# Kernel tuning notes

Hardware: AMD Instinct MI355X
Metric: run time of the kernel (lower is better)

Reference implementation:

```python
import jax, jax.numpy as jnp
import numpy as np

BS, N, M, E = 2, 512, 128, 16384
NNODE = BS * N
CI = CO = 32  # fused in-channels (16 skip + 16 upsampled), out-channels per degree


def _ln(x, g, b, eps=1e-5):
    mu = jnp.mean(x, -1, keepdims=True)
    var = jnp.var(x, -1, keepdims=True)
    return (x - mu) / jnp.sqrt(var + eps) * g + b


def reference(h0, h1, uph0, uph1, xyz, xyz_prev, r, basis_00, basis_01, basis_10, basis_11,
              rad_w1, rad_b1, rad_ln1_g, rad_ln1_b, rad_w2, rad_b2, rad_ln2_g, rad_ln2_b,
              rad_w3_00, rad_b3_00, rad_w3_01, rad_b3_01, rad_w3_10, rad_b3_10,
              rad_w3_11, rad_b3_11, self_w0, self_w1,
              norm_ln_g0, norm_ln_b0, norm_w0, norm_b0,
              norm_ln_g1, norm_ln_b1, norm_w1, norm_b1,
              edge_src, edge_dst):
    # ---- three_nn + inverse-squared-distance interpolation (upsample uph) ----
    xb = xyz.reshape(BS, N, 3)
    pb = xyz_prev.reshape(BS, M, 3)
    d2 = jnp.sum((xb[:, :, None, :] - pb[:, None, :, :]) ** 2, -1)  # [BS,N,M]
    neg, idx = jax.lax.top_k(-d2, 3)                                # 3 nearest prev points
    d2_3 = jnp.maximum(-neg, 1e-10)                                 # dist*dist with clamp
    inv = 1.0 / (d2_3 + 1e-8)
    w = inv / jnp.sum(inv, -1, keepdims=True)                       # [BS,N,3]
    w = jax.lax.stop_gradient(w)  # three_nn is a non-differentiable custom op in torch

    def interp(up, skip):
        nC, nF = up.shape[1], up.shape[2]
        flat = up.reshape(BS, M, nC * nF)
        g = jax.vmap(lambda f, i: f[i])(flat, idx)                  # [BS,N,3,nC*nF]
        new = jnp.sum(g * w[..., None], axis=2).reshape(BS * N, nC, nF)
        return jnp.concatenate([new, skip], axis=1)                 # upsampled first, then skip

    f0 = interp(uph0, h0)  # [NNODE, 32, 1]
    f1 = interp(uph1, h1)  # [NNODE, 32, 3]

    # ---- GConvSE3: radial nets (hidden trunk stacked over the 4 (di,do) pairs) ----
    hh = jnp.einsum('poi,ei->peo', rad_w1, r) + rad_b1[:, None, :]
    hh = jax.nn.relu(_ln(hh, rad_ln1_g[:, None, :], rad_ln1_b[:, None, :]))
    hh = jnp.einsum('poi,pei->peo', rad_w2, hh) + rad_b2[:, None, :]
    hh = jax.nn.relu(_ln(hh, rad_ln2_g[:, None, :], rad_ln2_b[:, None, :]))  # [4,E,32]

    def rad_out(p, w3, b3, f):
        y = hh[p] @ w3.T + b3
        return y.reshape(E, CO, CI, f)  # (out, in, freq) per RadialFunc.view

    R00 = rad_out(0, rad_w3_00, rad_b3_00, 1)
    R01 = rad_out(1, rad_w3_01, rad_b3_01, 1)
    R10 = rad_out(2, rad_w3_10, rad_b3_10, 1)
    R11 = rad_out(3, rad_w3_11, rad_b3_11, 3)

    src0 = f0[edge_src]; src1 = f1[edge_src]
    dst0 = f0[edge_dst]; dst1 = f1[edge_dst]

    def pair_msg(R, basis, src):
        # kernel[e,o,mo,c,mi] = sum_f R[e,o,c,f] * basis[e,mo,mi,f]; msg = kernel @ src
        T = jnp.einsum('emnf,ecn->ecmf', basis, src)
        return jnp.einsum('eocf,ecmf->eom', R, T)

    msg0 = pair_msg(R00, basis_00, src0) + pair_msg(R10, basis_10, src1)
    msg1 = pair_msg(R01, basis_01, src0) + pair_msg(R11, basis_11, src1)
    # per-edge self-interaction on the destination features
    msg0 = msg0 + jnp.einsum('oc,ecm->eom', self_w0, dst0)
    msg1 = msg1 + jnp.einsum('oc,ecm->eom', self_w1, dst1)

    deg = jnp.maximum(jax.ops.segment_sum(jnp.ones((E,), msg0.dtype), edge_dst, num_segments=NNODE), 1.0)
    out0 = jax.ops.segment_sum(msg0, edge_dst, num_segments=NNODE) / deg[:, None, None]
    out1 = jax.ops.segment_sum(msg1, edge_dst, num_segments=NNODE) / deg[:, None, None]

    # ---- GNormSE3: norm-gated nonlinearity (LayerNorm -> ReLU -> Linear on norms) ----
    def gnorm(v, g, b, wlin, blin):
        nrm = jnp.maximum(jnp.linalg.norm(v, axis=-1, keepdims=True), 1e-12)
        phase = v / nrm
        t = jax.nn.relu(_ln(nrm[..., 0], g, b)) @ wlin.T + blin
        return t[..., None] * phase

    out0 = gnorm(out0, norm_ln_g0, norm_ln_b0, norm_w0, norm_b0)  # [NNODE,32,1]
    out1 = gnorm(out1, norm_ln_g1, norm_ln_b1, norm_w1, norm_b1)  # [NNODE,32,3]
    return jnp.concatenate([out0, out1], axis=-1)                 # [NNODE,32,4]


def setup_inputs() -> dict:
    key = jax.random.key(0)
    ks = iter(jax.random.split(key, 64))
    def rn(shape, scale=1.0):
        return jax.random.normal(next(ks), shape, dtype=jnp.float32) * scale
    inp = {}
    inp['h0'] = rn((NNODE, 16, 1))
    inp['h1'] = rn((NNODE, 16, 3))
    inp['uph0'] = rn((BS * M, 16, 1))
    inp['uph1'] = rn((BS * M, 16, 3))
    inp['xyz'] = rn((NNODE, 3))
    inp['xyz_prev'] = rn((BS * M, 3))
    inp['r'] = jax.random.uniform(next(ks), (E, 1), dtype=jnp.float32, minval=0.05, maxval=2.0)
    inp['basis_00'] = rn((E, 1, 1, 1))
    inp['basis_01'] = rn((E, 3, 1, 1))
    inp['basis_10'] = rn((E, 1, 3, 1))
    inp['basis_11'] = rn((E, 3, 3, 3))
    inp['rad_w1'] = rn((4, 32, 1))
    inp['rad_b1'] = jnp.zeros((4, 32), jnp.float32)
    inp['rad_ln1_g'] = jnp.ones((4, 32), jnp.float32)
    inp['rad_ln1_b'] = jnp.zeros((4, 32), jnp.float32)
    inp['rad_w2'] = rn((4, 32, 32), 1.0 / np.sqrt(32))
    inp['rad_b2'] = jnp.zeros((4, 32), jnp.float32)
    inp['rad_ln2_g'] = jnp.ones((4, 32), jnp.float32)
    inp['rad_ln2_b'] = jnp.zeros((4, 32), jnp.float32)
    for nm, f in (('00', 1), ('01', 1), ('10', 1), ('11', 3)):
        inp['rad_w3_' + nm] = rn((f * CI * CO, 32), 1.0 / np.sqrt(32))
        inp['rad_b3_' + nm] = jnp.zeros((f * CI * CO,), jnp.float32)
    inp['self_w0'] = rn((CO, CI), 1.0 / np.sqrt(CI))
    inp['self_w1'] = rn((CO, CI), 1.0 / np.sqrt(CI))
    for d in ('0', '1'):
        inp['norm_ln_g' + d] = jnp.ones((CO,), jnp.float32)
        inp['norm_ln_b' + d] = jnp.zeros((CO,), jnp.float32)
        inp['norm_w' + d] = rn((CO, CO), 1.0 / np.sqrt(CO))
        inp['norm_b' + d] = jnp.zeros((CO,), jnp.float32)
    inp['edge_src'] = jax.random.randint(next(ks), (E,), 0, NNODE, dtype=jnp.int32)
    inp['edge_dst'] = jax.random.randint(next(ks), (E,), 0, NNODE, dtype=jnp.int32)
    return inp
```

## Files before the change

kernel.cpp:

```cpp
#include <hip/hip_runtime.h>

#define NNODE 1024
#define NPT   512
#define MPT   128
#define ETOT  16384


__global__ void zero_kernel(float* __restrict__ p) {
    const int i = blockIdx.x * 256 + threadIdx.x;
    if (i < 33024) ((float4*)p)[i] = make_float4(0.f, 0.f, 0.f, 0.f);
}

__global__ void interp_kernel(const float* __restrict__ h0, const float* __restrict__ h1,
                              const float* __restrict__ uph0, const float* __restrict__ uph1,
                              const float* __restrict__ xyz, const float* __restrict__ xyzp,
                              float* __restrict__ f0, float* __restrict__ f1) {
    __shared__ float sd2[128];
    __shared__ float sw[3];
    __shared__ int   sidx[3];
    const int n = blockIdx.x;
    const int t = threadIdx.x;
    const int b = n >> 9;
    const float x = xyz[n*3+0], y = xyz[n*3+1], z = xyz[n*3+2];
    const float* pb = &xyzp[(b*MPT + t)*3];
    const float dx = x - pb[0], dy = y - pb[1], dz = z - pb[2];
    sd2[t] = dx*dx + dy*dy + dz*dz;
    __syncthreads();
    if (t == 0) {
        float bd0 = 3.4e38f, bd1 = 3.4e38f, bd2 = 3.4e38f;
        int   i0 = 0, i1 = 0, i2 = 0;
        for (int i = 0; i < 128; ++i) {
            const float d = sd2[i];
            if (d < bd0)      { bd2 = bd1; i2 = i1; bd1 = bd0; i1 = i0; bd0 = d; i0 = i; }
            else if (d < bd1) { bd2 = bd1; i2 = i1; bd1 = d;   i1 = i; }
            else if (d < bd2) { bd2 = d;   i2 = i; }
        }
        const float inv0 = 1.f / (fmaxf(bd0, 1e-10f) + 1e-8f);
        const float inv1 = 1.f / (fmaxf(bd1, 1e-10f) + 1e-8f);
        const float inv2 = 1.f / (fmaxf(bd2, 1e-10f) + 1e-8f);
        const float s = inv0 + inv1 + inv2;
        sw[0] = inv0 / s; sw[1] = inv1 / s; sw[2] = inv2 / s;
        sidx[0] = i0; sidx[1] = i1; sidx[2] = i2;
    }
    __syncthreads();
    const float w0 = sw[0], w1 = sw[1], w2 = sw[2];
    const int g0 = b*MPT + sidx[0], g1 = b*MPT + sidx[1], g2 = b*MPT + sidx[2];
    if (t < 32) {
        const int c = t;
        float v;
        if (c < 16) v = w0*uph0[g0*16+c] + w1*uph0[g1*16+c] + w2*uph0[g2*16+c];
        else        v = h0[n*16 + (c-16)];
        f0[n*32 + c] = v;
    } else {
        const int q = t - 32, c = q / 3, m = q - c*3;
        float v;
        if (c < 16) v = w0*uph1[(g0*16+c)*3+m] + w1*uph1[(g1*16+c)*3+m] + w2*uph1[(g2*16+c)*3+m];
        else        v = h1[(n*16 + (c-16))*3 + m];
        f1[n*96 + c*3 + m] = v;
    }
}

__global__ void trunk_kernel(const float* __restrict__ r,
                             const float* __restrict__ w1, const float* __restrict__ b1,
                             const float* __restrict__ g1, const float* __restrict__ be1,
                             const float* __restrict__ w2, const float* __restrict__ b2,
                             const float* __restrict__ g2, const float* __restrict__ be2,
                             float* __restrict__ hh) {
    const int tid = blockIdx.x * 256 + threadIdx.x;
    const int p = tid >> 14, e = tid & 16383;
    const float rv = r[e];
    float a[32];
    float mu = 0.f;
    #pragma unroll
    for (int o = 0; o < 32; ++o) { a[o] = w1[p*32+o]*rv + b1[p*32+o]; mu += a[o]; }
    mu *= (1.f/32.f);
    float var = 0.f;
    #pragma unroll
    for (int o = 0; o < 32; ++o) { const float d = a[o]-mu; var += d*d; }
    var *= (1.f/32.f);
    float rs = 1.f / sqrtf(var + 1e-5f);
    float h[32];
    #pragma unroll
    for (int o = 0; o < 32; ++o)
        h[o] = fmaxf((a[o]-mu)*rs*g1[p*32+o] + be1[p*32+o], 0.f);
    float a2[32];
    mu = 0.f;
    #pragma unroll
    for (int o = 0; o < 32; ++o) {
        float acc = b2[p*32+o];
        const float* wr = &w2[(p*32+o)*32];
        #pragma unroll
        for (int i = 0; i < 32; ++i) acc += wr[i]*h[i];
        a2[o] = acc; mu += acc;
    }
    mu *= (1.f/32.f);
    var = 0.f;
    #pragma unroll
    for (int o = 0; o < 32; ++o) { const float d = a2[o]-mu; var += d*d; }
    var *= (1.f/32.f);
    rs = 1.f / sqrtf(var + 1e-5f);
    float outv[32];
    #pragma unroll
    for (int o = 0; o < 32; ++o)
        outv[o] = fmaxf((a2[o]-mu)*rs*g2[p*32+o] + be2[p*32+o], 0.f);
    float4* hv = (float4*)&hh[tid*32];
    #pragma unroll
    for (int j = 0; j < 8; ++j)
        hv[j] = make_float4(outv[j*4+0], outv[j*4+1], outv[j*4+2], outv[j*4+3]);
}

struct SmemMsg {
    float w3[32*132];
    float b3[32*5];
    float hh[32*36];
    float src0[32*36];
    float src1[32*100];
    float bas11[32*28];
    float T10[32*33];
    float T11[32*13];
    float bas00[32];
    float bas01[96];
    float bas10[96];
    int   dst[32];
};

template<int P>
__device__ __forceinline__ void process_pair(SmemMsg& sm, const float* __restrict__ hhg,
                                             const float* __restrict__ w3, const float* __restrict__ b3g,
                                             int e0, int tid, int o, int et,
                                             float (&msg0)[4], float (&msg1)[4][3],
                                             const float (&b00r)[4]) {
    constexpr int RPO = (P == 3) ? 96 : 32;
    __syncthreads();
    {
        const int i = tid >> 3, q = tid & 7;
        ((float4*)&sm.hh[i*36])[q] = ((const float4*)&hhg[((P << 14) + e0 + i)*32])[q];
    }
    __syncthreads();
    float4 hhr[4][8];
    #pragma unroll
    for (int ei = 0; ei < 4; ++ei)
        #pragma unroll
        for (int kq = 0; kq < 8; ++kq)
            hhr[ei][kq] = *(const float4*)&sm.hh[(et*4+ei)*36 + kq*4];
    float S01[4] = {0.f, 0.f, 0.f, 0.f};
    constexpr int NCH = RPO / 4;
    #pragma unroll 1
    for (int ch = 0; ch < NCH; ++ch) {
        const int r0 = ch*4;
        __syncthreads();
        {
            const int oo = tid >> 3, hq = tid & 7, rr = hq >> 1, hf = hq & 1;
            const int jrow = oo*RPO + r0 + rr;
            const float4* gs = (const float4*)&w3[jrow*32 + hf*16];
            float4* ld = (float4*)&sm.w3[oo*132 + rr*32 + hf*16];
            #pragma unroll
            for (int j = 0; j < 4; ++j) ld[j] = gs[j];
            if (hq < 4) sm.b3[oo*5 + hq] = b3g[oo*RPO + r0 + hq];
        }
        if (P == 3 && tid < 128) {
            const int e = tid >> 2, rr = tid & 3;
            const int cf = r0 + rr, c = cf / 3, fi = cf - c*3;
            #pragma unroll
            for (int m = 0; m < 3; ++m)
                sm.T11[e*13 + rr*3 + m] =
                      sm.bas11[e*28 + m*9 + 0 + fi] * sm.src1[e*100 + c*3 + 0]
                    + sm.bas11[e*28 + m*9 + 3 + fi] * sm.src1[e*100 + c*3 + 1]
                    + sm.bas11[e*28 + m*9 + 6 + fi] * sm.src1[e*100 + c*3 + 2];
        }
        __syncthreads();
        #pragma unroll
        for (int rr = 0; rr < 4; ++rr) {
            const int row = r0 + rr;
            float4 w[8];
            #pragma unroll
            for (int kq = 0; kq < 8; ++kq)
                w[kq] = *(const float4*)&sm.w3[o*132 + rr*32 + kq*4];
            const float bias = sm.b3[o*5 + rr];
            #pragma unroll
            for (int ei = 0; ei < 4; ++ei) {
                const int eL = et*4 + ei;
                float a0 = bias, a1 = 0.f, a2 = 0.f, a3 = 0.f;
                #pragma unroll
                for (int kq = 0; kq < 8; ++kq) {
                    a0 += w[kq].x * hhr[ei][kq].x;
                    a1 += w[kq].y * hhr[ei][kq].y;
                    a2 += w[kq].z * hhr[ei][kq].z;
                    a3 += w[kq].w * hhr[ei][kq].w;
                }
                const float R = (a0 + a1) + (a2 + a3);
                if (P == 0)      msg0[ei] += R * (b00r[ei] * sm.src0[eL*36 + row]);
                else if (P == 1) S01[ei]  += R * sm.src0[eL*36 + row];
                else if (P == 2) msg0[ei] += R * sm.T10[eL*33 + row];
                else {
                    #pragma unroll
                    for (int m = 0; m < 3; ++m)
                        msg1[ei][m] += R * sm.T11[eL*13 + rr*3 + m];
                }
            }
        }
    }
    if (P == 1) {
        #pragma unroll
        for (int ei = 0; ei < 4; ++ei)
            #pragma unroll
            for (int m = 0; m < 3; ++m)
                msg1[ei][m] += S01[ei] * sm.bas01[(et*4+ei)*3 + m];
    }
}

__launch_bounds__(256, 2)
__global__ void msg_kernel(const float* __restrict__ hhg,
                           const float* __restrict__ f0g, const float* __restrict__ f1g,
                           const float* __restrict__ w00, const float* __restrict__ b00g,
                           const float* __restrict__ w01, const float* __restrict__ b01g,
                           const float* __restrict__ w10, const float* __restrict__ b10g,
                           const float* __restrict__ w11, const float* __restrict__ b11g,
                           const float* __restrict__ bas00g, const float* __restrict__ bas01g,
                           const float* __restrict__ bas10g, const float* __restrict__ bas11g,
                           const int* __restrict__ esrc, const int* __restrict__ edst,
                           float* __restrict__ acc0, float* __restrict__ acc1,
                           float* __restrict__ deg) {
    __shared__ SmemMsg sm;
    const int tid = threadIdx.x;
    const int o = tid & 31, et = tid >> 5;
    const int e0 = blockIdx.x * 32;
    {
        const int i = tid >> 3, q = tid & 7;
        const int eg = e0 + i;
        const int s = esrc[eg];
        ((float4*)&sm.src0[i*36])[q] = ((const float4*)&f0g[s*32])[q];
        #pragma unroll
        for (int j = 0; j < 3; ++j)
            ((float4*)&sm.src1[i*100])[q + 8*j] = ((const float4*)&f1g[s*96])[q + 8*j];
        #pragma unroll
        for (int j = 0; j < 4; ++j) {
            const int idx = q*4 + j;
            if (idx < 27) sm.bas11[i*28 + idx] = bas11g[eg*27 + idx];
        }
        if (q == 0) sm.bas00[i] = bas00g[eg];
        if (q == 1) sm.dst[i] = edst[eg];
        if (q < 3)  sm.bas01[i*3 + q] = bas01g[eg*3 + q];
        if (q >= 4 && q < 7) sm.bas10[i*3 + q - 4] = bas10g[eg*3 + q - 4];
    }
    __syncthreads();
    if (tid < 32) atomicAdd(&deg[sm.dst[tid]], 1.0f);
    {
        #pragma unroll
        for (int j = 0; j < 4; ++j) {
            const int id = tid + 256*j;
            const int e = id >> 5, c = id & 31;
            sm.T10[e*33 + c] = sm.bas10[e*3+0]*sm.src1[e*100 + c*3 + 0]
                             + sm.bas10[e*3+1]*sm.src1[e*100 + c*3 + 1]
                             + sm.bas10[e*3+2]*sm.src1[e*100 + c*3 + 2];
        }
    }
    float msg0[4] = {0.f, 0.f, 0.f, 0.f};
    float msg1[4][3] = {{0,0,0},{0,0,0},{0,0,0},{0,0,0}};
    float b00r[4];
    #pragma unroll
    for (int ei = 0; ei < 4; ++ei) b00r[ei] = sm.bas00[et*4 + ei];

    process_pair<0>(sm, hhg, w00, b00g, e0, tid, o, et, msg0, msg1, b00r);
    process_pair<1>(sm, hhg, w01, b01g, e0, tid, o, et, msg0, msg1, b00r);
    process_pair<2>(sm, hhg, w10, b10g, e0, tid, o, et, msg0, msg1, b00r);
    process_pair<3>(sm, hhg, w11, b11g, e0, tid, o, et, msg0, msg1, b00r);

    #pragma unroll
    for (int ei = 0; ei < 4; ++ei) {
        const int d = sm.dst[et*4 + ei];
        atomicAdd(&acc0[d*32 + o], msg0[ei]);
        #pragma unroll
        for (int m = 0; m < 3; ++m)
            atomicAdd(&acc1[(d*32 + o)*3 + m], msg1[ei][m]);
    }
}

__launch_bounds__(256)
__global__ void epi_kernel(const float* __restrict__ acc0, const float* __restrict__ acc1,
                           const float* __restrict__ deg,
                           const float* __restrict__ f0, const float* __restrict__ f1,
                           const float* __restrict__ sw0, const float* __restrict__ sw1,
                           const float* __restrict__ g0v, const float* __restrict__ b0v,
                           const float* __restrict__ nw0, const float* __restrict__ nb0,
                           const float* __restrict__ g1v, const float* __restrict__ b1v,
                           const float* __restrict__ nw1, const float* __restrict__ nb1,
                           float* __restrict__ out) {
    __shared__ float s_sw0[1024], s_sw1[1024], s_nw0[1024], s_nw1[1024];
    __shared__ float s_act0[8][33], s_act1[8][33];
    const int tid = threadIdx.x;
    #pragma unroll
    for (int j = 0; j < 4; ++j) {
        s_sw0[tid + 256*j] = sw0[tid + 256*j];
        s_sw1[tid + 256*j] = sw1[tid + 256*j];
        s_nw0[tid + 256*j] = nw0[tid + 256*j];
        s_nw1[tid + 256*j] = nw1[tid + 256*j];
    }
    const int o = tid & 31, nl = tid >> 5;
    const int n = blockIdx.x * 8 + nl;
    const float dr = deg[n];
    const float dc = fmaxf(dr, 1.0f);
    float v0 = acc0[n*32 + o] / dc;
    float v1[3];
    #pragma unroll
    for (int m = 0; m < 3; ++m) v1[m] = acc1[(n*32 + o)*3 + m] / dc;
    __syncthreads();
    if (dr > 0.f) {
        #pragma unroll
        for (int c = 0; c < 32; ++c) {
            v0 += s_sw0[o*32 + c] * f0[n*32 + c];
            const float w1c = s_sw1[o*32 + c];
            #pragma unroll
            for (int m = 0; m < 3; ++m) v1[m] += w1c * f1[(n*32 + c)*3 + m];
        }
    }
    const float nrm0 = fmaxf(fabsf(v0), 1e-12f);
    const float nrm1 = fmaxf(sqrtf(v1[0]*v1[0] + v1[1]*v1[1] + v1[2]*v1[2]), 1e-12f);
    float mu0 = nrm0, mu1 = nrm1;
    #pragma unroll
    for (int msk = 16; msk >= 1; msk >>= 1) { mu0 += __shfl_xor(mu0, msk); mu1 += __shfl_xor(mu1, msk); }
    mu0 *= (1.f/32.f); mu1 *= (1.f/32.f);
    const float d0 = nrm0 - mu0, d1 = nrm1 - mu1;
    float s0 = d0*d0, s1 = d1*d1;
    #pragma unroll
    for (int msk = 16; msk >= 1; msk >>= 1) { s0 += __shfl_xor(s0, msk); s1 += __shfl_xor(s1, msk); }
    const float var0 = s0*(1.f/32.f), var1 = s1*(1.f/32.f);
    const float a0 = fmaxf(d0 / sqrtf(var0 + 1e-5f) * g0v[o] + b0v[o], 0.f);
    const float a1 = fmaxf(d1 / sqrtf(var1 + 1e-5f) * g1v[o] + b1v[o], 0.f);
    s_act0[nl][o] = a0; s_act1[nl][o] = a1;
    __syncthreads();
    float t0 = nb0[o], t1 = nb1[o];
    #pragma unroll
    for (int c = 0; c < 32; ++c) {
        t0 += s_act0[nl][c] * s_nw0[o*32 + c];
        t1 += s_act1[nl][c] * s_nw1[o*32 + c];
    }
    float4 ov;
    ov.x = t0 * (v0 / nrm0);
    ov.y = t1 * (v1[0] / nrm1);
    ov.z = t1 * (v1[1] / nrm1);
    ov.w = t1 * (v1[2] / nrm1);
    *(float4*)&out[(n*32 + o)*4] = ov;
}

extern "C" void kernel_launch(void* const* d_in, const int* in_sizes, int n_in,
                              void* d_out, int out_size, void* d_ws, size_t ws_size,
                              hipStream_t stream) {
    const float* h0    = (const float*)d_in[0];
    const float* h1    = (const float*)d_in[1];
    const float* uph0  = (const float*)d_in[2];
    const float* uph1  = (const float*)d_in[3];
    const float* xyz   = (const float*)d_in[4];
    const float* xyzp  = (const float*)d_in[5];
    const float* r     = (const float*)d_in[6];
    const float* bas00 = (const float*)d_in[7];
    const float* bas01 = (const float*)d_in[8];
    const float* bas10 = (const float*)d_in[9];
    const float* bas11 = (const float*)d_in[10];
    const float* rw1   = (const float*)d_in[11];
    const float* rb1   = (const float*)d_in[12];
    const float* rg1   = (const float*)d_in[13];
    const float* rbe1  = (const float*)d_in[14];
    const float* rw2   = (const float*)d_in[15];
    const float* rb2   = (const float*)d_in[16];
    const float* rg2   = (const float*)d_in[17];
    const float* rbe2  = (const float*)d_in[18];
    const float* w00   = (const float*)d_in[19];
    const float* b00   = (const float*)d_in[20];
    const float* w01   = (const float*)d_in[21];
    const float* b01   = (const float*)d_in[22];
    const float* w10   = (const float*)d_in[23];
    const float* b10   = (const float*)d_in[24];
    const float* w11   = (const float*)d_in[25];
    const float* b11   = (const float*)d_in[26];
    const float* sw0   = (const float*)d_in[27];
    const float* sw1   = (const float*)d_in[28];
    const float* g0    = (const float*)d_in[29];
    const float* bb0   = (const float*)d_in[30];
    const float* nw0   = (const float*)d_in[31];
    const float* nb0   = (const float*)d_in[32];
    const float* g1    = (const float*)d_in[33];
    const float* bb1   = (const float*)d_in[34];
    const float* nw1   = (const float*)d_in[35];
    const float* nb1   = (const float*)d_in[36];
    const int*   esrc  = (const int*)d_in[37];
    const int*   edst  = (const int*)d_in[38];

    float* ws   = (float*)d_ws;
    float* f0   = ws;
    float* f1   = ws + 32768;
    float* hh   = ws + 131072;
    float* acc0 = ws + 2228224;
    float* acc1 = ws + 2260992;
    float* degb = ws + 2359296;
    float* out  = (float*)d_out;

    zero_kernel<<<129, 256, 0, stream>>>(acc0);
    interp_kernel<<<1024, 128, 0, stream>>>(h0, h1, uph0, uph1, xyz, xyzp, f0, f1);
    trunk_kernel<<<256, 256, 0, stream>>>(r, rw1, rb1, rg1, rbe1, rw2, rb2, rg2, rbe2, hh);
    msg_kernel<<<512, 256, 0, stream>>>(hh, f0, f1, w00, b00, w01, b01, w10, b10, w11, b11,
                                        bas00, bas01, bas10, bas11, esrc, edst, acc0, acc1, degb);
    epi_kernel<<<128, 256, 0, stream>>>(acc0, acc1, degb, f0, f1, sw0, sw1,
                                        g0, bb0, nw0, nb0, g1, bb1, nw1, nb1, out);
}
```

Measured before the change: 659.0 us.

## Restructure message kernel as per-wave work items with edge-per-lane dot products

Rewrites the message kernel so that each wavefront owns 64 edges and one of seven work slices: pair 00, pair 01, pair 10, or one of four output-channel groups of pair 11. Each lane computes its own radial-weight dot products, reading w3 rows at wave-uniform addresses (scalar/broadcast loads) instead of staging them through LDS with many block-wide barriers. This removes shared-memory staging and synchronisation, but each lane does far more serial work and holds 32-plus accumulators in registers. The number of atomics also grows, because pair 01 now adds straight into acc1 and each wave writes its results separately.

```diff
diff --git a/kernel.cpp b/kernel.cpp
--- a/kernel.cpp
+++ b/kernel.cpp
@@ -109,170 +109,141 @@
         hv[j] = make_float4(outv[j*4+0], outv[j*4+1], outv[j*4+2], outv[j*4+3]);
 }
 
-struct SmemMsg {
-    float w3[32*132];
-    float b3[32*5];
-    float hh[32*36];
-    float src0[32*36];
-    float src1[32*100];
-    float bas11[32*28];
-    float T10[32*33];
-    float T11[32*13];
-    float bas00[32];
-    float bas01[96];
-    float bas10[96];
-    int   dst[32];
-};
-
-template<int P>
-__device__ __forceinline__ void process_pair(SmemMsg& sm, const float* __restrict__ hhg,
-                                             const float* __restrict__ w3, const float* __restrict__ b3g,
-                                             int e0, int tid, int o, int et,
-                                             float (&msg0)[4], float (&msg1)[4][3],
-                                             const float (&b00r)[4]) {
-    constexpr int RPO = (P == 3) ? 96 : 32;
-    __syncthreads();
-    {
-        const int i = tid >> 3, q = tid & 7;
-        ((float4*)&sm.hh[i*36])[q] = ((const float4*)&hhg[((P << 14) + e0 + i)*32])[q];
-    }
-    __syncthreads();
-    float4 hhr[4][8];
-    #pragma unroll
-    for (int ei = 0; ei < 4; ++ei)
-        #pragma unroll
-        for (int kq = 0; kq < 8; ++kq)
-            hhr[ei][kq] = *(const float4*)&sm.hh[(et*4+ei)*36 + kq*4];
-    float S01[4] = {0.f, 0.f, 0.f, 0.f};
-    constexpr int NCH = RPO / 4;
-    #pragma unroll 1
-    for (int ch = 0; ch < NCH; ++ch) {
-        const int r0 = ch*4;
-        __syncthreads();
-        {
-            const int oo = tid >> 3, hq = tid & 7, rr = hq >> 1, hf = hq & 1;
-            const int jrow = oo*RPO + r0 + rr;
-            const float4* gs = (const float4*)&w3[jrow*32 + hf*16];
-            float4* ld = (float4*)&sm.w3[oo*132 + rr*32 + hf*16];
-            #pragma unroll
-            for (int j = 0; j < 4; ++j) ld[j] = gs[j];
-            if (hq < 4) sm.b3[oo*5 + hq] = b3g[oo*RPO + r0 + hq];
-        }
-        if (P == 3 && tid < 128) {
-            const int e = tid >> 2, rr = tid & 3;
-            const int cf = r0 + rr, c = cf / 3, fi = cf - c*3;
-            #pragma unroll
-            for (int m = 0; m < 3; ++m)
-                sm.T11[e*13 + rr*3 + m] =
-                      sm.bas11[e*28 + m*9 + 0 + fi] * sm.src1[e*100 + c*3 + 0]
-                    + sm.bas11[e*28 + m*9 + 3 + fi] * sm.src1[e*100 + c*3 + 1]
-                    + sm.bas11[e*28 + m*9 + 6 + fi] * sm.src1[e*100 + c*3 + 2];
-        }
-        __syncthreads();
-        #pragma unroll
-        for (int rr = 0; rr < 4; ++rr) {
-            const int row = r0 + rr;
-            float4 w[8];
-            #pragma unroll
-            for (int kq = 0; kq < 8; ++kq)
-                w[kq] = *(const float4*)&sm.w3[o*132 + rr*32 + kq*4];
-            const float bias = sm.b3[o*5 + rr];
-            #pragma unroll
-            for (int ei = 0; ei < 4; ++ei) {
-                const int eL = et*4 + ei;
-                float a0 = bias, a1 = 0.f, a2 = 0.f, a3 = 0.f;
-                #pragma unroll
-                for (int kq = 0; kq < 8; ++kq) {
-                    a0 += w[kq].x * hhr[ei][kq].x;
-                    a1 += w[kq].y * hhr[ei][kq].y;
-                    a2 += w[kq].z * hhr[ei][kq].z;
-                    a3 += w[kq].w * hhr[ei][kq].w;
-                }
-                const float R = (a0 + a1) + (a2 + a3);
-                if (P == 0)      msg0[ei] += R * (b00r[ei] * sm.src0[eL*36 + row]);
-                else if (P == 1) S01[ei]  += R * sm.src0[eL*36 + row];
-                else if (P == 2) msg0[ei] += R * sm.T10[eL*33 + row];
-                else {
-                    #pragma unroll
-                    for (int m = 0; m < 3; ++m)
-                        msg1[ei][m] += R * sm.T11[eL*13 + rr*3 + m];
-                }
-            }
-        }
-    }
-    if (P == 1) {
-        #pragma unroll
-        for (int ei = 0; ei < 4; ++ei)
-            #pragma unroll
-            for (int m = 0; m < 3; ++m)
-                msg1[ei][m] += S01[ei] * sm.bas01[(et*4+ei)*3 + m];
-    }
+__device__ __forceinline__ float dot32b(const float* __restrict__ wr,
+                                        const float* __restrict__ h, float bias) {
+    float a0 = bias, a1 = 0.f, a2 = 0.f, a3 = 0.f;
+    #pragma unroll
+    for (int k = 0; k < 32; k += 4) {
+        a0 = fmaf(wr[k+0], h[k+0], a0);
+        a1 = fmaf(wr[k+1], h[k+1], a1);
+        a2 = fmaf(wr[k+2], h[k+2], a2);
+        a3 = fmaf(wr[k+3], h[k+3], a3);
+    }
+    return (a0 + a1) + (a2 + a3);
 }
 
 __launch_bounds__(256, 2)
 __global__ void msg_kernel(const float* __restrict__ hhg,
                            const float* __restrict__ f0g, const float* __restrict__ f1g,
-                           const float* __restrict__ w00, const float* __restrict__ b00g,
-                           const float* __restrict__ w01, const float* __restrict__ b01g,
-                           const float* __restrict__ w10, const float* __restrict__ b10g,
-                           const float* __restrict__ w11, const float* __restrict__ b11g,
+                           const float* __restrict__ w3_00, const float* __restrict__ b3_00,
+                           const float* __restrict__ w3_01, const float* __restrict__ b3_01,
+                           const float* __restrict__ w3_10, const float* __restrict__ b3_10,
+                           const float* __restrict__ w3_11, const float* __restrict__ b3_11,
                            const float* __restrict__ bas00g, const float* __restrict__ bas01g,
                            const float* __restrict__ bas10g, const float* __restrict__ bas11g,
                            const int* __restrict__ esrc, const int* __restrict__ edst,
                            float* __restrict__ acc0, float* __restrict__ acc1,
                            float* __restrict__ deg) {
-    __shared__ SmemMsg sm;
-    const int tid = threadIdx.x;
-    const int o = tid & 31, et = tid >> 5;
-    const int e0 = blockIdx.x * 32;
+    const int lane = threadIdx.x & 63;
+    const int W = __builtin_amdgcn_readfirstlane(blockIdx.x * 4 + (threadIdx.x >> 6));
+    const int g = W / 7;
+    const int q = W - g * 7;
+    const int e = (g << 6) + lane;
+    const int s = esrc[e];
+    const int d = edst[e];
+
+    float hh[32];
     {
-        const int i = tid >> 3, q = tid & 7;
-        const int eg = e0 + i;
-        const int s = esrc[eg];
-        ((float4*)&sm.src0[i*36])[q] = ((const float4*)&f0g[s*32])[q];
-        #pragma unroll
-        for (int j = 0; j < 3; ++j)
-            ((float4*)&sm.src1[i*100])[q + 8*j] = ((const float4*)&f1g[s*96])[q + 8*j];
-        #pragma unroll
-        for (int j = 0; j < 4; ++j) {
-            const int idx = q*4 + j;
-            if (idx < 27) sm.bas11[i*28 + idx] = bas11g[eg*27 + idx];
-        }
-        if (q == 0) sm.bas00[i] = bas00g[eg];
-        if (q == 1) sm.dst[i] = edst[eg];
-        if (q < 3)  sm.bas01[i*3 + q] = bas01g[eg*3 + q];
-        if (q >= 4 && q < 7) sm.bas10[i*3 + q - 4] = bas10g[eg*3 + q - 4];
-    }
-    __syncthreads();
-    if (tid < 32) atomicAdd(&deg[sm.dst[tid]], 1.0f);
-    {
-        #pragma unroll
-        for (int j = 0; j < 4; ++j) {
-            const int id = tid + 256*j;
-            const int e = id >> 5, c = id & 31;
-            sm.T10[e*33 + c] = sm.bas10[e*3+0]*sm.src1[e*100 + c*3 + 0]
-                             + sm.bas10[e*3+1]*sm.src1[e*100 + c*3 + 1]
-                             + sm.bas10[e*3+2]*sm.src1[e*100 + c*3 + 2];
-        }
-    }
-    float msg0[4] = {0.f, 0.f, 0.f, 0.f};
-    float msg1[4][3] = {{0,0,0},{0,0,0},{0,0,0},{0,0,0}};
-    float b00r[4];
-    #pragma unroll
-    for (int ei = 0; ei < 4; ++ei) b00r[ei] = sm.bas00[et*4 + ei];
-
-    process_pair<0>(sm, hhg, w00, b00g, e0, tid, o, et, msg0, msg1, b00r);
-    process_pair<1>(sm, hhg, w01, b01g, e0, tid, o, et, msg0, msg1, b00r);
-    process_pair<2>(sm, hhg, w10, b10g, e0, tid, o, et, msg0, msg1, b00r);
-    process_pair<3>(sm, hhg, w11, b11g, e0, tid, o, et, msg0, msg1, b00r);
-
-    #pragma unroll
-    for (int ei = 0; ei < 4; ++ei) {
-        const int d = sm.dst[et*4 + ei];
-        atomicAdd(&acc0[d*32 + o], msg0[ei]);
-        #pragma unroll
-        for (int m = 0; m < 3; ++m)
-            atomicAdd(&acc1[(d*32 + o)*3 + m], msg1[ei][m]);
+        const int p = (q < 2) ? q : ((q == 2) ? 2 : 3);
+        const float4* hv = (const float4*)&hhg[((p << 14) + e) << 5];
+        #pragma unroll
+        for (int j = 0; j < 8; ++j) {
+            float4 v = hv[j];
+            hh[j*4] = v.x; hh[j*4+1] = v.y; hh[j*4+2] = v.z; hh[j*4+3] = v.w;
+        }
+    }
+
+    if (q < 2) {
+        const float* hw = (q == 0) ? w3_00 : w3_01;
+        const float* hb = (q == 0) ? b3_00 : b3_01;
+        const float scale = (q == 0) ? bas00g[e] : 1.0f;
+        if (q == 0) atomicAdd(&deg[d], 1.0f);
+        float acc[32];
+        #pragma unroll
+        for (int o = 0; o < 32; ++o) acc[o] = 0.f;
+        float srcv = f0g[s << 5];
+        #pragma unroll 1
+        for (int c = 0; c < 32; ++c) {
+            const float nxt = (c < 31) ? f0g[(s << 5) + c + 1] : 0.f;
+            const float pre = scale * srcv;
+            #pragma unroll
+            for (int o = 0; o < 32; ++o) {
+                const int row = (o << 5) + c;
+                const float R = dot32b(&hw[row << 5], hh, hb[row]);
+                acc[o] = fmaf(R, pre, acc[o]);
+            }
+            srcv = nxt;
+        }
+        if (q == 0) {
+            #pragma unroll
+            for (int o = 0; o < 32; ++o) atomicAdd(&acc0[(d << 5) + o], acc[o]);
+        } else {
+            const float bm0 = bas01g[e*3], bm1 = bas01g[e*3+1], bm2 = bas01g[e*3+2];
+            #pragma unroll
+            for (int o = 0; o < 32; ++o) {
+                const int base = ((d << 5) + o) * 3;
+                atomicAdd(&acc1[base+0], acc[o] * bm0);
+                atomicAdd(&acc1[base+1], acc[o] * bm1);
+                atomicAdd(&acc1[base+2], acc[o] * bm2);
+            }
+        }
+    } else if (q == 2) {
+        const float bn0 = bas10g[e*3], bn1 = bas10g[e*3+1], bn2 = bas10g[e*3+2];
+        float acc[32];
+        #pragma unroll
+        for (int o = 0; o < 32; ++o) acc[o] = 0.f;
+        float s0 = f1g[s*96+0], s1v = f1g[s*96+1], s2 = f1g[s*96+2];
+        #pragma unroll 1
+        for (int c = 0; c < 32; ++c) {
+            float n0 = 0.f, n1 = 0.f, n2 = 0.f;
+            if (c < 31) { n0 = f1g[s*96+c*3+3]; n1 = f1g[s*96+c*3+4]; n2 = f1g[s*96+c*3+5]; }
+            const float pre = bn0*s0 + bn1*s1v + bn2*s2;
+            #pragma unroll
+            for (int o = 0; o < 32; ++o) {
+                const int row = (o << 5) + c;
+                const float R = dot32b(&w3_10[row << 5], hh, b3_10[row]);
+                acc[o] = fmaf(R, pre, acc[o]);
+            }
+            s0 = n0; s1v = n1; s2 = n2;
+        }
+        #pragma unroll
+        for (int o = 0; o < 32; ++o) atomicAdd(&acc0[(d << 5) + o], acc[o]);
+    } else {
+        const int ob = (q - 3) << 3;
+        float bas[27];
+        #pragma unroll
+        for (int i = 0; i < 27; ++i) bas[i] = bas11g[e*27 + i];
+        float acc[8][3];
+        #pragma unroll
+        for (int oo = 0; oo < 8; ++oo) { acc[oo][0] = 0.f; acc[oo][1] = 0.f; acc[oo][2] = 0.f; }
+        float s0 = f1g[s*96+0], s1v = f1g[s*96+1], s2 = f1g[s*96+2];
+        #pragma unroll 1
+        for (int c = 0; c < 32; ++c) {
+            float n0 = 0.f, n1 = 0.f, n2 = 0.f;
+            if (c < 31) { n0 = f1g[s*96+c*3+3]; n1 = f1g[s*96+c*3+4]; n2 = f1g[s*96+c*3+5]; }
+            #pragma unroll
+            for (int fi = 0; fi < 3; ++fi) {
+                const float t0 = bas[0+0*3+fi]*s0 + bas[0+1*3+fi]*s1v + bas[0+2*3+fi]*s2;
+                const float t1 = bas[9+0*3+fi]*s0 + bas[9+1*3+fi]*s1v + bas[9+2*3+fi]*s2;
+                const float t2 = bas[18+0*3+fi]*s0 + bas[18+1*3+fi]*s1v + bas[18+2*3+fi]*s2;
+                #pragma unroll
+                for (int oo = 0; oo < 8; ++oo) {
+                    const int row = (ob + oo)*96 + c*3 + fi;
+                    const float R = dot32b(&w3_11[row << 5], hh, b3_11[row]);
+                    acc[oo][0] = fmaf(R, t0, acc[oo][0]);
+                    acc[oo][1] = fmaf(R, t1, acc[oo][1]);
+                    acc[oo][2] = fmaf(R, t2, acc[oo][2]);
+                }
+            }
+            s0 = n0; s1v = n1; s2 = n2;
+        }
+        #pragma unroll
+        for (int oo = 0; oo < 8; ++oo) {
+            const int base = ((d << 5) + ob + oo) * 3;
+            atomicAdd(&acc1[base+0], acc[oo][0]);
+            atomicAdd(&acc1[base+1], acc[oo][1]);
+            atomicAdd(&acc1[base+2], acc[oo][2]);
+        }
     }
 }
 
@@ -398,7 +369,7 @@
     zero_kernel<<<129, 256, 0, stream>>>(acc0);
     interp_kernel<<<1024, 128, 0, stream>>>(h0, h1, uph0, uph1, xyz, xyzp, f0, f1);
     trunk_kernel<<<256, 256, 0, stream>>>(r, rw1, rb1, rg1, rbe1, rw2, rb2, rg2, rbe2, hh);
-    msg_kernel<<<512, 256, 0, stream>>>(hh, f0, f1, w00, b00, w01, b01, w10, b10, w11, b11,
+    msg_kernel<<<448, 256, 0, stream>>>(hh, f0, f1, w00, b00, w01, b01, w10, b10, w11, b11,
                                         bas00, bas01, bas10, bas11, esrc, edst, acc0, acc1, degb);
     epi_kernel<<<128, 256, 0, stream>>>(acc0, acc1, degb, f0, f1, sw0, sw1,
                                         g0, bb0, nw0, nb0, g1, bb1, nw1, nb1, out);
```

Result: slower. 685.3 us (+4.0%).
